# Kernel optimization log

Measured on AMD Instinct MI355X. Metric: run time of the kernel, lower is better.

The kernel has to match this reference:

```python
import jax, jax.numpy as jnp
import numpy as np

B, S, E, H, DK, DV = 2, 2048, 1024, 16, 64, 64
NEG = -1e9


def setup_inputs() -> dict:
    key = jax.random.key(0)
    ks = jax.random.split(key, 12)
    s = 0.02
    return {
        "query": jax.random.normal(ks[0], (B, S, E), jnp.float32),
        "key": jax.random.normal(ks[1], (B, S, E), jnp.float32),
        "value": jax.random.normal(ks[2], (B, S, E), jnp.float32),
        "mask": jax.random.randint(ks[3], (B, S, S), 0, 2, jnp.int32),
        "Wq": jax.random.normal(ks[4], (E, H * DK), jnp.float32) * s,
        "bq": jnp.zeros((H * DK,), jnp.float32),
        "Wk": jax.random.normal(ks[5], (E, H * DK), jnp.float32) * s,
        "bk": jnp.zeros((H * DK,), jnp.float32),
        "Wv": jax.random.normal(ks[6], (E, H * DV), jnp.float32) * s,
        "bv": jnp.zeros((H * DV,), jnp.float32),
        "Wo": jax.random.normal(ks[7], (H * DV, E), jnp.float32) * s,
        "bo": jnp.zeros((E,), jnp.float32),
    }


def reference(query, key, value, mask, Wq, bq, Wk, bk, Wv, bv, Wo, bo):
    # projections, then split heads: (B,S,H*D) -> (B,H,S,D)
    q = (query @ Wq + bq).reshape(B, S, H, DK).transpose(0, 2, 1, 3)
    k = (key @ Wk + bk).reshape(B, S, H, DK).transpose(0, 2, 1, 3)
    v = (value @ Wv + bv).reshape(B, S, H, DV).transpose(0, 2, 1, 3)
    scores = jnp.einsum("bhqd,bhkd->bhqk", q, k) / jnp.sqrt(jnp.float32(DK))
    scores = jnp.where(mask[:, None, :, :] == 0, jnp.float32(NEG), scores)
    weights = jax.nn.softmax(scores, axis=-1)
    ctx = jnp.einsum("bhqk,bhkd->bhqd", weights, v)
    ctx = ctx.transpose(0, 2, 1, 3).reshape(B, S, H * DV)
    return ctx @ Wo + bo
```

## Files before the change

### kernel.cpp

```cpp
#include <hip/hip_runtime.h>

typedef __attribute__((ext_vector_type(8))) short s16x8;
typedef __attribute__((ext_vector_type(4))) float f32x4;
typedef __attribute__((ext_vector_type(16))) float f32x16;
typedef unsigned short u16;
typedef unsigned int u32;
typedef unsigned long long u64;

__device__ __forceinline__ u16 f2bf(float f) {
  u32 u = __builtin_bit_cast(u32, f);
  u += 0x7fff + ((u >> 16) & 1);
  return (u16)(u >> 16);
}

__device__ __forceinline__ float exp2fast(float x) {
#if __has_builtin(__builtin_amdgcn_exp2f)
  return __builtin_amdgcn_exp2f(x);
#else
  return __expf(x * 0.6931471805599453f);
#endif
}

__device__ __forceinline__ void gload16(const void* g, void* l) {
  __builtin_amdgcn_global_load_lds((const __attribute__((address_space(1))) u32*)g,
                                   (__attribute__((address_space(3))) u32*)l, 16, 0, 0);
}

#define MFMA(a, b, c) __builtin_amdgcn_mfma_f32_16x16x32_bf16((a), (b), (c), 0, 0, 0)
#define MFMA32(a, b, c) __builtin_amdgcn_mfma_f32_32x32x16_bf16((a), (b), (c), 0, 0, 0)

#define QSCALE 0.18033688011112042f

__global__ __launch_bounds__(256) void prep(
    const float* __restrict__ q, const float* __restrict__ k, const float* __restrict__ v,
    u16* __restrict__ oq, u16* __restrict__ ok, u16* __restrict__ ov,
    const float* __restrict__ W0, const float* __restrict__ W1,
    const float* __restrict__ W2, const float* __restrict__ W3,
    u16* __restrict__ T0, u16* __restrict__ T1, u16* __restrict__ T2, u16* __restrict__ T3,
    const int* __restrict__ mask, u64* __restrict__ mb) {
  __shared__ float t[32][33];
  const int bx = blockIdx.x, tid = threadIdx.x;
  if (bx < 6144) {
    int z = bx >> 11;
    const float* src = (z == 0) ? q : (z == 1) ? k : v;
    u16* dst = (z == 0) ? oq : (z == 1) ? ok : ov;
    int i = (bx & 2047) * 256 + tid;
    const float4* s4 = (const float4*)src;
    float4 a = s4[2 * i], bb = s4[2 * i + 1];
    uint4 o;
    o.x = (u32)f2bf(a.x) | ((u32)f2bf(a.y) << 16);
    o.y = (u32)f2bf(a.z) | ((u32)f2bf(a.w) << 16);
    o.z = (u32)f2bf(bb.x) | ((u32)f2bf(bb.y) << 16);
    o.w = (u32)f2bf(bb.z) | ((u32)f2bf(bb.w) << 16);
    ((uint4*)dst)[i] = o;
  } else if (bx < 10240) {
    int r = bx - 6144;
    int z = r >> 10, t2 = r & 1023;
    const float* W = (z == 0) ? W0 : (z == 1) ? W1 : (z == 2) ? W2 : W3;
    u16* WT = (z == 0) ? T0 : (z == 1) ? T1 : (z == 2) ? T2 : T3;
    int nb = t2 & 31, kb = t2 >> 5;
    int tx = tid & 31, ty = tid >> 5;
    int n = nb * 32 + tx;
#pragma unroll
    for (int j = 0; j < 4; j++) {
      int kk = kb * 32 + ty + 8 * j;
      t[ty + 8 * j][tx] = W[(size_t)kk * 1024 + n];
    }
    __syncthreads();
    int kk = kb * 32 + tx;
#pragma unroll
    for (int j = 0; j < 4; j++) {
      int n2 = nb * 32 + ty + 8 * j;
      WT[(size_t)n2 * 1024 + kk] = f2bf(t[tx][ty + 8 * j]);
    }
  } else {
    int wi = (bx - 10240) * 4 + (tid >> 6);
    int lane = tid & 63;
    u64 bits = __ballot(mask[((size_t)wi << 6) + lane] != 0);
    if (lane == 0) mb[wi] = bits;
  }
}

template <int BM, int BN>
__device__ __forceinline__ void gemm_core(const u16* __restrict__ A, const u16* __restrict__ BT,
                                          int m0, int n0, u16* Ash, u16* Bsh,
                                          f32x4 (&acc)[BM / 32][BN / 32]) {
  constexpr int MF = BM / 32, NF = BN / 32;
  constexpr int BATCH = BM / 32 + BN / 32;
  const int tid = threadIdx.x;
  const int lane = tid & 63, wid = tid >> 6;
  const int r16 = lane & 15, g = lane >> 4;
  const int wm = wid >> 1, wn = wid & 1;
  const int swz = r16 & 7;
  const f32x4 vz = {0.f, 0.f, 0.f, 0.f};
#pragma unroll
  for (int mf = 0; mf < MF; mf++)
#pragma unroll
    for (int nf = 0; nf < NF; nf++) acc[mf][nf] = vz;

  auto stage = [&](int buf, int k0) {
#pragma unroll
    for (int i = 0; i < MF; i++) {
      int ch = i * 256 + tid;
      int row = ch >> 3, sc = (ch & 7) ^ (row & 7);
      gload16(A + (((size_t)(m0 + row)) << 10) + k0 + sc * 8,
              Ash + (size_t)buf * (BM * 64) + ch * 8);
    }
#pragma unroll
    for (int i = 0; i < NF; i++) {
      int ch = i * 256 + tid;
      int row = ch >> 3, sc = (ch & 7) ^ (row & 7);
      gload16(BT + (((size_t)(n0 + row)) << 10) + k0 + sc * 8,
              Bsh + (size_t)buf * (BN * 64) + ch * 8);
    }
  };

  asm volatile("" ::: "memory");
  stage(0, 0);
  asm volatile("" ::: "memory");
  stage(1, 64);
  asm volatile("" ::: "memory");

  for (int t = 0; t < 16; t++) {
    const int cur = t & 1;
    if (t == 15) {
      asm volatile("s_waitcnt vmcnt(0)" ::: "memory");
    } else if constexpr (BATCH == 8) {
      asm volatile("s_waitcnt vmcnt(8)" ::: "memory");
    } else {
      asm volatile("s_waitcnt vmcnt(6)" ::: "memory");
    }
    asm volatile("s_barrier" ::: "memory");

    const u16* Acur = Ash + (size_t)cur * (BM * 64);
    const u16* Bcur = Bsh + (size_t)cur * (BN * 64);
    __builtin_amdgcn_s_setprio(1);
#pragma unroll
    for (int kk = 0; kk < 2; kk++) {
      const int c = (kk * 4 + g);
      s16x8 af[MF], bfr[NF];
#pragma unroll
      for (int mf = 0; mf < MF; mf++)
        af[mf] = *(const s16x8*)(Acur + ((wm * (BM / 2) + mf * 16 + r16) << 6) +
                                 ((c ^ swz) << 3));
#pragma unroll
      for (int nf = 0; nf < NF; nf++)
        bfr[nf] = *(const s16x8*)(Bcur + ((wn * (BN / 2) + nf * 16 + r16) << 6) +
                                  ((c ^ swz) << 3));
#pragma unroll
      for (int mf = 0; mf < MF; mf++)
#pragma unroll
        for (int nf = 0; nf < NF; nf++) acc[mf][nf] = MFMA(af[mf], bfr[nf], acc[mf][nf]);
    }
    __builtin_amdgcn_s_setprio(0);

    asm volatile("s_barrier" ::: "memory");
    if (t + 2 < 16) stage(cur, (t + 2) * 64);
  }
}

__global__ __launch_bounds__(256, 2) void proj_gemm(
    const u16* __restrict__ Xq, const u16* __restrict__ Xk, const u16* __restrict__ Xv,
    const u16* __restrict__ WqT, const u16* __restrict__ WkT, const u16* __restrict__ WvT,
    const float* __restrict__ bq, const float* __restrict__ bk, const float* __restrict__ bv,
    u16* __restrict__ Qo, u16* __restrict__ Ko, u16* __restrict__ Vto) {
  __shared__ u16 Ash[2 * 128 * 64], Bsh[2 * 128 * 64];
  const int z = blockIdx.z;
  const u16* A = (z == 0) ? Xq : (z == 1) ? Xk : Xv;
  const u16* BT = (z == 0) ? WqT : (z == 1) ? WkT : WvT;
  const float* bias = (z == 0) ? bq : (z == 1) ? bk : bv;
  u16* O = (z == 0) ? Qo : (z == 1) ? Ko : Vto;
  const float sc = (z == 0) ? QSCALE : 1.0f;
  const int m0 = blockIdx.y * 128, n0 = blockIdx.x * 128;
  f32x4 acc[4][4];
  gemm_core<128, 128>(A, BT, m0, n0, Ash, Bsh, acc);
  const int tid = threadIdx.x, lane = tid & 63, wid = tid >> 6;
  const int r16 = lane & 15, g = lane >> 4, wm = wid >> 1, wn = wid & 1;
#pragma unroll
  for (int nf = 0; nf < 4; nf++) {
    int col = n0 + wn * 64 + nf * 16 + r16;
    float bb = bias[col];
    int h = col >> 6, d = col & 63;
#pragma unroll
    for (int mf = 0; mf < 4; mf++) {
#pragma unroll
      for (int ri = 0; ri < 4; ri++) {
        int row = m0 + wm * 64 + mf * 16 + g * 4 + ri;
        int b_ = row >> 11, s_ = row & 2047;
        u16 val = f2bf((acc[mf][nf][ri] + bb) * sc);
        if (z < 2)
          O[((((size_t)b_ * 16 + h) * 2048 + s_) << 6) + d] = val;
        else
          O[((((size_t)b_ * 16 + h) * 64 + d) << 11) + s_] = val;
      }
    }
  }
}

__global__ __launch_bounds__(256, 2) void out_gemm(const u16* __restrict__ ctx,
                                                   const u16* __restrict__ WoT,
                                                   const float* __restrict__ bo,
                                                   float* __restrict__ out) {
  __shared__ u16 Ash[2 * 64 * 64], Bsh[2 * 128 * 64];
  const int m0 = blockIdx.y * 64, n0 = blockIdx.x * 128;
  f32x4 acc[2][4];
  gemm_core<64, 128>(ctx, WoT, m0, n0, Ash, Bsh, acc);
  const int tid = threadIdx.x, lane = tid & 63, wid = tid >> 6;
  const int r16 = lane & 15, g = lane >> 4, wm = wid >> 1, wn = wid & 1;
#pragma unroll
  for (int nf = 0; nf < 4; nf++) {
    int col = n0 + wn * 64 + nf * 16 + r16;
    float bb = bo[col];
#pragma unroll
    for (int mf = 0; mf < 2; mf++) {
#pragma unroll
      for (int ri = 0; ri < 4; ri++) {
        int row = m0 + wm * 32 + mf * 16 + g * 4 + ri;
        out[((size_t)row << 10) + col] = acc[mf][nf][ri] + bb;
      }
    }
  }
}

__device__ __forceinline__ s16x8 pack4u(u32 a0, u32 a1, u32 b0, u32 b1) {
  union { u32 u[4]; s16x8 v; } p;
  p.u[0] = a0; p.u[1] = a1; p.u[2] = b0; p.u[3] = b1;
  return p.v;
}

__device__ __forceinline__ void softpack(const f32x16& sv, u32 wm, s16x8& pA, s16x8& pB) {
  float e[16];
#pragma unroll
  for (int qd = 0; qd < 4; qd++)
#pragma unroll
    for (int j = 0; j < 4; j++) {
      const int bit = qd * 8 + j;
      float ex = exp2fast(sv[qd * 4 + j]);
      u32 sext = (u32)(((int)(wm << (31 - bit))) >> 31);
      e[qd * 4 + j] = __builtin_bit_cast(float, __builtin_bit_cast(u32, ex) & sext);
    }
#pragma unroll
  for (int n = 0; n < 2; n++) {
    u32 a0, a1, b0, b1;
    asm("v_cvt_pk_bf16_f32 %0, %1, %2" : "=v"(a0) : "v"(e[n * 8 + 0]), "v"(e[n * 8 + 1]));
    asm("v_cvt_pk_bf16_f32 %0, %1, %2" : "=v"(a1) : "v"(e[n * 8 + 2]), "v"(e[n * 8 + 3]));
    asm("v_cvt_pk_bf16_f32 %0, %1, %2" : "=v"(b0) : "v"(e[n * 8 + 4]), "v"(e[n * 8 + 5]));
    asm("v_cvt_pk_bf16_f32 %0, %1, %2" : "=v"(b1) : "v"(e[n * 8 + 6]), "v"(e[n * 8 + 7]));
    asm("v_permlane32_swap_b32 %0, %1" : "+v"(a0), "+v"(b0));
    asm("v_permlane32_swap_b32 %0, %1" : "+v"(a1), "+v"(b1));
    if (n == 0) pA = pack4u(a0, a1, b0, b1);
    else        pB = pack4u(a0, a1, b0, b1);
  }
}

__global__ __launch_bounds__(256, 2) void flash_attn(const u16* __restrict__ Q,
                                                     const u16* __restrict__ K,
                                                     const u16* __restrict__ Vt,
                                                     const u64* __restrict__ Mb64,
                                                     u16* __restrict__ ctx) {
  __shared__ __align__(16) u16 Ksh[4][64][64];
  __shared__ __align__(16) u16 Vsh[4][64][64];

  const int tid = threadIdx.x, w = tid >> 6, lane = tid & 63;
  const int l31 = lane & 31, h5 = lane >> 5, l7 = lane & 7;

  int work = ((int)blockIdx.x & 7) * 64 + ((int)blockIdx.x >> 3);
  const int qt = work & 15, bh = work >> 4;
  const int b = bh >> 4, h = bh & 15;
  const int q0 = qt * 128 + w * 32;

  const u16* Qb = Q + ((size_t)bh << 17);
  const u16* Kb = K + ((size_t)bh << 17);
  const u16* Vb = Vt + ((size_t)bh << 17);
  const u64* Mrow = Mb64 + ((size_t)(b * 2048 + q0 + l31) << 5);

  const int srow = tid >> 3, sk16 = tid & 7;
#define STAGE(buf, kv0)                                                                   \
  {                                                                                       \
    _Pragma("unroll") for (int i = 0; i < 2; i++) {                                       \
      int row = i * 32 + srow;                                                            \
      int sc = sk16 ^ (row & 7);                                                          \
      gload16(Kb + (((size_t)((kv0) + row)) << 6) + sc * 8,                               \
              (char*)&Ksh[buf][0][0] + (i * 256 + tid) * 16);                             \
      gload16(Vb + (((size_t)row) << 11) + (kv0) + sc * 8,                                \
              (char*)&Vsh[buf][0][0] + (i * 256 + tid) * 16);                             \
    }                                                                                     \
  }

  s16x8 aq[4];
#pragma unroll
  for (int dk = 0; dk < 4; dk++)
    aq[dk] = *(const s16x8*)(Qb + ((q0 + l31) << 6) + dk * 16 + h5 * 8);
  asm volatile("" ::: "memory");
  STAGE(0, 0);
  STAGE(1, 64);
  u64 m_c0 = Mrow[0], m_c1 = Mrow[1];
  asm volatile("" ::: "memory");
  STAGE(2, 128);
  STAGE(3, 192);
  u64 m_n0 = Mrow[2], m_n1 = Mrow[3];
  asm volatile("" ::: "memory");

  s16x8 vones;
#pragma unroll
  for (int j = 0; j < 8; j++) vones[j] = (short)0x3F80;

  f32x16 o0, o1, o4;
#pragma unroll
  for (int r = 0; r < 16; r++) { o0[r] = 0.f; o1[r] = 0.f; o4[r] = 0.f; }

  for (int t = 0; t < 16; t++) {
    const int base = (t & 1) * 2;
    if (t == 15) {
      asm volatile("s_waitcnt vmcnt(0)" ::: "memory");
    } else {
      asm volatile("s_waitcnt vmcnt(10)" ::: "memory");
    }
    asm volatile("s_barrier" ::: "memory");

    const u16* KcA = &Ksh[base][0][0];
    const u16* KcB = &Ksh[base + 1][0][0];
    const u16* VcA = &Vsh[base][0][0];
    const u16* VcB = &Vsh[base + 1][0][0];

    f32x16 s0, s1, s2, s3;
#pragma unroll
    for (int r = 0; r < 16; r++) { s0[r] = 0.f; s1[r] = 0.f; s2[r] = 0.f; s3[r] = 0.f; }
    __builtin_amdgcn_s_setprio(1);
#pragma unroll
    for (int dk = 0; dk < 4; dk++) {
      int ch = (((dk << 1) + h5) ^ l7) << 3;
      s16x8 akA0 = *(const s16x8*)(KcA + (l31 << 6) + ch);
      s16x8 akA1 = *(const s16x8*)(KcA + ((32 + l31) << 6) + ch);
      s16x8 akB0 = *(const s16x8*)(KcB + (l31 << 6) + ch);
      s16x8 akB1 = *(const s16x8*)(KcB + ((32 + l31) << 6) + ch);
      s0 = MFMA32(akA0, aq[dk], s0);
      s1 = MFMA32(akA1, aq[dk], s1);
      s2 = MFMA32(akB0, aq[dk], s2);
      s3 = MFMA32(akB1, aq[dk], s3);
    }
    __builtin_amdgcn_s_setprio(0);

    u64 mshA = m_c0 >> (h5 << 2);
    s16x8 pa[4];
    softpack(s0, (u32)mshA, pa[0], pa[1]);
    softpack(s1, (u32)(mshA >> 32), pa[2], pa[3]);
    __builtin_amdgcn_s_setprio(1);
#pragma unroll
    for (int km = 0; km < 4; km++) {
      int ch = (((km << 1) + h5) ^ l7) << 3;
      s16x8 bv0 = *(const s16x8*)(VcA + (l31 << 6) + ch);
      s16x8 bv1 = *(const s16x8*)(VcA + ((32 + l31) << 6) + ch);
      o0 = MFMA32(pa[km], bv0, o0);
      o1 = MFMA32(pa[km], bv1, o1);
      o4 = MFMA32(pa[km], vones, o4);
    }
    __builtin_amdgcn_s_setprio(0);

    u64 mshB = m_c1 >> (h5 << 2);
    s16x8 pb[4];
    softpack(s2, (u32)mshB, pb[0], pb[1]);
    softpack(s3, (u32)(mshB >> 32), pb[2], pb[3]);
    __builtin_amdgcn_s_setprio(1);
#pragma unroll
    for (int km = 0; km < 4; km++) {
      int ch = (((km << 1) + h5) ^ l7) << 3;
      s16x8 bv0 = *(const s16x8*)(VcB + (l31 << 6) + ch);
      s16x8 bv1 = *(const s16x8*)(VcB + ((32 + l31) << 6) + ch);
      o0 = MFMA32(pb[km], bv0, o0);
      o1 = MFMA32(pb[km], bv1, o1);
      o4 = MFMA32(pb[km], vones, o4);
    }
    __builtin_amdgcn_s_setprio(0);

    asm volatile("s_barrier" ::: "memory");
    u64 mw0 = 0, mw1 = 0;
    if (t + 2 < 16) {
      STAGE(base, (2 * t + 4) * 64);
      STAGE(base + 1, (2 * t + 5) * 64);
      mw0 = Mrow[2 * t + 4];
      mw1 = Mrow[2 * t + 5];
    }
    m_c0 = m_n0; m_c1 = m_n1;
    m_n0 = mw0;  m_n1 = mw1;
  }
#undef STAGE

#pragma unroll
  for (int r = 0; r < 16; r++) {
    int qr = (r & 3) + 8 * (r >> 2) + 4 * h5;
    size_t rowoff = ((size_t)((b << 11) + q0 + qr)) << 10;
    float iv = 1.f / o4[r];
    ctx[rowoff + (h << 6) + l31]      = f2bf(o0[r] * iv);
    ctx[rowoff + (h << 6) + 32 + l31] = f2bf(o1[r] * iv);
  }
}

extern "C" void kernel_launch(void* const* d_in, const int* in_sizes, int n_in,
                              void* d_out, int out_size, void* d_ws, size_t ws_size,
                              hipStream_t stream) {
  const float* query = (const float*)d_in[0];
  const float* key_  = (const float*)d_in[1];
  const float* value = (const float*)d_in[2];
  const int*   mask  = (const int*)d_in[3];
  const float* Wq = (const float*)d_in[4];
  const float* bq = (const float*)d_in[5];
  const float* Wk = (const float*)d_in[6];
  const float* bk = (const float*)d_in[7];
  const float* Wv = (const float*)d_in[8];
  const float* bv = (const float*)d_in[9];
  const float* Wo = (const float*)d_in[10];
  const float* bo = (const float*)d_in[11];

  const size_t MB = 1048576;
  char* ws = (char*)d_ws;
  u16* Xq  = (u16*)(ws + 0 * MB);
  u16* Xk  = (u16*)(ws + 8 * MB);
  u16* Xv  = (u16*)(ws + 16 * MB);
  u16* WqT = (u16*)(ws + 24 * MB);
  u16* WkT = (u16*)(ws + 26 * MB);
  u16* WvT = (u16*)(ws + 28 * MB);
  u16* WoT = (u16*)(ws + 30 * MB);
  u16* Qd  = (u16*)(ws + 32 * MB);
  u16* Kd  = (u16*)(ws + 40 * MB);
  u16* Vtd = (u16*)(ws + 48 * MB);
  u16* ctx = (u16*)(ws + 56 * MB);
  u64* Mb  = (u64*)(ws + 72 * MB);

  prep<<<43008, 256, 0, stream>>>(query, key_, value, Xq, Xk, Xv,
                                  Wq, Wk, Wv, Wo, WqT, WkT, WvT, WoT, mask, Mb);

  proj_gemm<<<dim3(8, 32, 3), 256, 0, stream>>>(Xq, Xk, Xv, WqT, WkT, WvT, bq, bk, bv,
                                                Qd, Kd, Vtd);
  flash_attn<<<512, 256, 0, stream>>>(Qd, Kd, Vtd, Mb, ctx);
  out_gemm<<<dim3(8, 64), 256, 0, stream>>>(ctx, WoT, bo, (float*)d_out);
}
```

Baseline: 152.0 us.

## Split KV range across two wave groups per block with LDS partial reduction

Flash attention blocks now run 512 threads: two groups of four waves each process half of the KV sequence for the same 128 query rows, each with its own double-buffered K/V LDS region. The unnormalized partial outputs and row sums are combined through LDS before the final normalize-and-store. The mask bitmap layout is transposed so that each tile's mask words for consecutive query rows sit contiguously. This roughly doubles resident waves to hide latency, at the cost of a cross-group reduction, more LDS per block, and a shallower prefetch.

```diff
diff --git a/kernel.cpp b/kernel.cpp
--- a/kernel.cpp
+++ b/kernel.cpp
@@ -77,7 +77,10 @@
     int wi = (bx - 10240) * 4 + (tid >> 6);
     int lane = tid & 63;
     u64 bits = __ballot(mask[((size_t)wi << 6) + lane] != 0);
-    if (lane == 0) mb[wi] = bits;
+    if (lane == 0) {
+      int b_ = wi >> 16, q_ = (wi >> 5) & 2047, t_ = wi & 31;
+      mb[((size_t)b_ << 16) + ((size_t)t_ << 11) + q_] = bits;
+    }
   }
 }
 
@@ -253,37 +256,42 @@
   }
 }
 
-__global__ __launch_bounds__(256, 2) void flash_attn(const u16* __restrict__ Q,
+__global__ __launch_bounds__(512, 4) void flash_attn(const u16* __restrict__ Q,
                                                      const u16* __restrict__ K,
                                                      const u16* __restrict__ Vt,
                                                      const u64* __restrict__ Mb64,
                                                      u16* __restrict__ ctx) {
-  __shared__ __align__(16) u16 Ksh[4][64][64];
-  __shared__ __align__(16) u16 Vsh[4][64][64];
-
+  __shared__ __align__(16) char pool[65536];
   const int tid = threadIdx.x, w = tid >> 6, lane = tid & 63;
   const int l31 = lane & 31, h5 = lane >> 5, l7 = lane & 7;
+  const int g4 = w >> 2;
+  const int gt = tid & 255;
+
+  u16* Ksh = (u16*)(pool + g4 * 32768);
+  u16* Vsh = (u16*)(pool + g4 * 32768 + 16384);
 
   int work = ((int)blockIdx.x & 7) * 64 + ((int)blockIdx.x >> 3);
   const int qt = work & 15, bh = work >> 4;
   const int b = bh >> 4, h = bh & 15;
-  const int q0 = qt * 128 + w * 32;
+  const int q0 = qt * 128 + (w & 3) * 32;
 
   const u16* Qb = Q + ((size_t)bh << 17);
   const u16* Kb = K + ((size_t)bh << 17);
   const u16* Vb = Vt + ((size_t)bh << 17);
-  const u64* Mrow = Mb64 + ((size_t)(b * 2048 + q0 + l31) << 5);
-
-  const int srow = tid >> 3, sk16 = tid & 7;
+  const u64* MrowT = Mb64 + ((size_t)b << 16) + (q0 + l31);
+  const int w0 = g4 * 16;
+  const int kvb = g4 * 1024;
+
+  const int srow = gt >> 3, sk16 = gt & 7;
 #define STAGE(buf, kv0)                                                                   \
   {                                                                                       \
     _Pragma("unroll") for (int i = 0; i < 2; i++) {                                       \
       int row = i * 32 + srow;                                                            \
       int sc = sk16 ^ (row & 7);                                                          \
       gload16(Kb + (((size_t)((kv0) + row)) << 6) + sc * 8,                               \
-              (char*)&Ksh[buf][0][0] + (i * 256 + tid) * 16);                             \
+              (char*)Ksh + ((buf) * 512 + i * 256 + gt) * 16);                            \
       gload16(Vb + (((size_t)row) << 11) + (kv0) + sc * 8,                                \
-              (char*)&Vsh[buf][0][0] + (i * 256 + tid) * 16);                             \
+              (char*)Vsh + ((buf) * 512 + i * 256 + gt) * 16);                            \
     }                                                                                     \
   }
 
@@ -292,13 +300,11 @@
   for (int dk = 0; dk < 4; dk++)
     aq[dk] = *(const s16x8*)(Qb + ((q0 + l31) << 6) + dk * 16 + h5 * 8);
   asm volatile("" ::: "memory");
-  STAGE(0, 0);
-  STAGE(1, 64);
-  u64 m_c0 = Mrow[0], m_c1 = Mrow[1];
-  asm volatile("" ::: "memory");
-  STAGE(2, 128);
-  STAGE(3, 192);
-  u64 m_n0 = Mrow[2], m_n1 = Mrow[3];
+  STAGE(0, kvb);
+  u64 m_c = MrowT[(size_t)(w0 + 0) << 11];
+  asm volatile("" ::: "memory");
+  STAGE(1, kvb + 64);
+  u64 m_n = MrowT[(size_t)(w0 + 1) << 11];
   asm volatile("" ::: "memory");
 
   s16x8 vones;
@@ -310,89 +316,89 @@
   for (int r = 0; r < 16; r++) { o0[r] = 0.f; o1[r] = 0.f; o4[r] = 0.f; }
 
   for (int t = 0; t < 16; t++) {
-    const int base = (t & 1) * 2;
+    const int cur = t & 1;
     if (t == 15) {
       asm volatile("s_waitcnt vmcnt(0)" ::: "memory");
     } else {
-      asm volatile("s_waitcnt vmcnt(10)" ::: "memory");
+      asm volatile("s_waitcnt vmcnt(5)" ::: "memory");
     }
     asm volatile("s_barrier" ::: "memory");
 
-    const u16* KcA = &Ksh[base][0][0];
-    const u16* KcB = &Ksh[base + 1][0][0];
-    const u16* VcA = &Vsh[base][0][0];
-    const u16* VcB = &Vsh[base + 1][0][0];
-
-    f32x16 s0, s1, s2, s3;
-#pragma unroll
-    for (int r = 0; r < 16; r++) { s0[r] = 0.f; s1[r] = 0.f; s2[r] = 0.f; s3[r] = 0.f; }
+    const u16* Kc = Ksh + cur * 4096;
+    const u16* Vc = Vsh + cur * 4096;
+
+    f32x16 s0, s1;
+#pragma unroll
+    for (int r = 0; r < 16; r++) { s0[r] = 0.f; s1[r] = 0.f; }
     __builtin_amdgcn_s_setprio(1);
 #pragma unroll
     for (int dk = 0; dk < 4; dk++) {
       int ch = (((dk << 1) + h5) ^ l7) << 3;
-      s16x8 akA0 = *(const s16x8*)(KcA + (l31 << 6) + ch);
-      s16x8 akA1 = *(const s16x8*)(KcA + ((32 + l31) << 6) + ch);
-      s16x8 akB0 = *(const s16x8*)(KcB + (l31 << 6) + ch);
-      s16x8 akB1 = *(const s16x8*)(KcB + ((32 + l31) << 6) + ch);
-      s0 = MFMA32(akA0, aq[dk], s0);
-      s1 = MFMA32(akA1, aq[dk], s1);
-      s2 = MFMA32(akB0, aq[dk], s2);
-      s3 = MFMA32(akB1, aq[dk], s3);
+      s16x8 ak0 = *(const s16x8*)(Kc + (l31 << 6) + ch);
+      s16x8 ak1 = *(const s16x8*)(Kc + ((32 + l31) << 6) + ch);
+      s0 = MFMA32(ak0, aq[dk], s0);
+      s1 = MFMA32(ak1, aq[dk], s1);
     }
     __builtin_amdgcn_s_setprio(0);
 
-    u64 mshA = m_c0 >> (h5 << 2);
+    u64 msh = m_c >> (h5 << 2);
     s16x8 pa[4];
-    softpack(s0, (u32)mshA, pa[0], pa[1]);
-    softpack(s1, (u32)(mshA >> 32), pa[2], pa[3]);
+    softpack(s0, (u32)msh, pa[0], pa[1]);
+    softpack(s1, (u32)(msh >> 32), pa[2], pa[3]);
+
     __builtin_amdgcn_s_setprio(1);
 #pragma unroll
     for (int km = 0; km < 4; km++) {
       int ch = (((km << 1) + h5) ^ l7) << 3;
-      s16x8 bv0 = *(const s16x8*)(VcA + (l31 << 6) + ch);
-      s16x8 bv1 = *(const s16x8*)(VcA + ((32 + l31) << 6) + ch);
+      s16x8 bv0 = *(const s16x8*)(Vc + (l31 << 6) + ch);
+      s16x8 bv1 = *(const s16x8*)(Vc + ((32 + l31) << 6) + ch);
       o0 = MFMA32(pa[km], bv0, o0);
       o1 = MFMA32(pa[km], bv1, o1);
       o4 = MFMA32(pa[km], vones, o4);
     }
     __builtin_amdgcn_s_setprio(0);
 
-    u64 mshB = m_c1 >> (h5 << 2);
-    s16x8 pb[4];
-    softpack(s2, (u32)mshB, pb[0], pb[1]);
-    softpack(s3, (u32)(mshB >> 32), pb[2], pb[3]);
-    __builtin_amdgcn_s_setprio(1);
-#pragma unroll
-    for (int km = 0; km < 4; km++) {
-      int ch = (((km << 1) + h5) ^ l7) << 3;
-      s16x8 bv0 = *(const s16x8*)(VcB + (l31 << 6) + ch);
-      s16x8 bv1 = *(const s16x8*)(VcB + ((32 + l31) << 6) + ch);
-      o0 = MFMA32(pb[km], bv0, o0);
-      o1 = MFMA32(pb[km], bv1, o1);
-      o4 = MFMA32(pb[km], vones, o4);
-    }
-    __builtin_amdgcn_s_setprio(0);
-
     asm volatile("s_barrier" ::: "memory");
-    u64 mw0 = 0, mw1 = 0;
+    u64 m_new = 0;
     if (t + 2 < 16) {
-      STAGE(base, (2 * t + 4) * 64);
-      STAGE(base + 1, (2 * t + 5) * 64);
-      mw0 = Mrow[2 * t + 4];
-      mw1 = Mrow[2 * t + 5];
-    }
-    m_c0 = m_n0; m_c1 = m_n1;
-    m_n0 = mw0;  m_n1 = mw1;
+      STAGE(cur, kvb + (t + 2) * 64);
+      m_new = MrowT[(size_t)(w0 + t + 2) << 11];
+    }
+    m_c = m_n;
+    m_n = m_new;
   }
 #undef STAGE
 
-#pragma unroll
-  for (int r = 0; r < 16; r++) {
-    int qr = (r & 3) + 8 * (r >> 2) + 4 * h5;
-    size_t rowoff = ((size_t)((b << 11) + q0 + qr)) << 10;
-    float iv = 1.f / o4[r];
-    ctx[rowoff + (h << 6) + l31]      = f2bf(o0[r] * iv);
-    ctx[rowoff + (h << 6) + 32 + l31] = f2bf(o1[r] * iv);
+  float* part = (float*)pool;
+  if (g4 == 1) {
+    float* dst = part + (((w & 3) * 64 + lane) * 48);
+#pragma unroll
+    for (int j = 0; j < 4; j++) {
+      *(float4*)(dst + j * 4)      = make_float4(o0[j * 4], o0[j * 4 + 1], o0[j * 4 + 2], o0[j * 4 + 3]);
+      *(float4*)(dst + 16 + j * 4) = make_float4(o1[j * 4], o1[j * 4 + 1], o1[j * 4 + 2], o1[j * 4 + 3]);
+      *(float4*)(dst + 32 + j * 4) = make_float4(o4[j * 4], o4[j * 4 + 1], o4[j * 4 + 2], o4[j * 4 + 3]);
+    }
+  }
+  __syncthreads();
+  if (g4 == 0) {
+    const float* src = part + (((w & 3) * 64 + lane) * 48);
+#pragma unroll
+    for (int j = 0; j < 4; j++) {
+      float4 p0 = *(const float4*)(src + j * 4);
+      float4 p1 = *(const float4*)(src + 16 + j * 4);
+      float4 p4 = *(const float4*)(src + 32 + j * 4);
+      o0[j * 4] += p0.x; o0[j * 4 + 1] += p0.y; o0[j * 4 + 2] += p0.z; o0[j * 4 + 3] += p0.w;
+      o1[j * 4] += p1.x; o1[j * 4 + 1] += p1.y; o1[j * 4 + 2] += p1.z; o1[j * 4 + 3] += p1.w;
+      o4[j * 4] += p4.x; o4[j * 4 + 1] += p4.y; o4[j * 4 + 2] += p4.z; o4[j * 4 + 3] += p4.w;
+    }
+#pragma unroll
+    for (int r = 0; r < 16; r++) {
+      int qr = (r & 3) + 8 * (r >> 2) + 4 * h5;
+      size_t rowoff = ((size_t)((b << 11) + q0 + qr)) << 10;
+      float iv = 1.f / o4[r];
+      ctx[rowoff + (h << 6) + l31]      = f2bf(o0[r] * iv);
+      ctx[rowoff + (h << 6) + 32 + l31] = f2bf(o1[r] * iv);
+    }
   }
 }
 
@@ -432,6 +438,6 @@
 
   proj_gemm<<<dim3(8, 32, 3), 256, 0, stream>>>(Xq, Xk, Xv, WqT, WkT, WvT, bq, bk, bv,
                                                 Qd, Kd, Vtd);
-  flash_attn<<<512, 256, 0, stream>>>(Qd, Kd, Vtd, Mb, ctx);
+  flash_attn<<<512, 512, 0, stream>>>(Qd, Kd, Vtd, Mb, ctx);
   out_gemm<<<dim3(8, 64), 256, 0, stream>>>(ctx, WoT, bo, (float*)d_out);
 }
```

Measured after the change: 153.6 us. About the same (+1.0%).

## Move mask bit-packing into projection GEMM launch with transposed bitmask layout

Applied to the files above, without the earlier changes.

Mask ballot packing moves out of the prep kernel into an extra z-slice of the projection GEMM grid, so it can run alongside the GEMM tiles. Each 256-thread block now loops over 128 mask words per wave. The packed mask is stored transposed (batch, kv-tile, query), so the per-lane mask loads in flash attention hit consecutive addresses and coalesce. The risk is that the mask blocks, which do little work per block, compete with GEMM blocks for CUs and that the longer per-block loop adds latency.

```diff
diff --git a/kernel.cpp b/kernel.cpp
--- a/kernel.cpp
+++ b/kernel.cpp
@@ -36,8 +36,7 @@
     u16* __restrict__ oq, u16* __restrict__ ok, u16* __restrict__ ov,
     const float* __restrict__ W0, const float* __restrict__ W1,
     const float* __restrict__ W2, const float* __restrict__ W3,
-    u16* __restrict__ T0, u16* __restrict__ T1, u16* __restrict__ T2, u16* __restrict__ T3,
-    const int* __restrict__ mask, u64* __restrict__ mb) {
+    u16* __restrict__ T0, u16* __restrict__ T1, u16* __restrict__ T2, u16* __restrict__ T3) {
   __shared__ float t[32][33];
   const int bx = blockIdx.x, tid = threadIdx.x;
   if (bx < 6144) {
@@ -53,7 +52,7 @@
     o.z = (u32)f2bf(bb.x) | ((u32)f2bf(bb.y) << 16);
     o.w = (u32)f2bf(bb.z) | ((u32)f2bf(bb.w) << 16);
     ((uint4*)dst)[i] = o;
-  } else if (bx < 10240) {
+  } else {
     int r = bx - 6144;
     int z = r >> 10, t2 = r & 1023;
     const float* W = (z == 0) ? W0 : (z == 1) ? W1 : (z == 2) ? W2 : W3;
@@ -73,11 +72,6 @@
       int n2 = nb * 32 + ty + 8 * j;
       WT[(size_t)n2 * 1024 + kk] = f2bf(t[tx][ty + 8 * j]);
     }
-  } else {
-    int wi = (bx - 10240) * 4 + (tid >> 6);
-    int lane = tid & 63;
-    u64 bits = __ballot(mask[((size_t)wi << 6) + lane] != 0);
-    if (lane == 0) mb[wi] = bits;
   }
 }
 
@@ -163,9 +157,24 @@
     const u16* __restrict__ Xq, const u16* __restrict__ Xk, const u16* __restrict__ Xv,
     const u16* __restrict__ WqT, const u16* __restrict__ WkT, const u16* __restrict__ WvT,
     const float* __restrict__ bq, const float* __restrict__ bk, const float* __restrict__ bv,
-    u16* __restrict__ Qo, u16* __restrict__ Ko, u16* __restrict__ Vto) {
+    u16* __restrict__ Qo, u16* __restrict__ Ko, u16* __restrict__ Vto,
+    const int* __restrict__ mask, u64* __restrict__ mb) {
   __shared__ u16 Ash[2 * 128 * 64], Bsh[2 * 128 * 64];
   const int z = blockIdx.z;
+  if (z == 3) {
+    int m = blockIdx.y * 8 + blockIdx.x;
+    int w = threadIdx.x >> 6, lane = threadIdx.x & 63;
+#pragma unroll 4
+    for (int j = 0; j < 128; j++) {
+      int wi = (m * 4 + w) * 128 + j;
+      u64 bits = __ballot(mask[((size_t)wi << 6) + lane] != 0);
+      if (lane == 0) {
+        int b_ = wi >> 16, q_ = (wi >> 5) & 2047, t_ = wi & 31;
+        mb[((size_t)b_ << 16) + ((size_t)t_ << 11) + q_] = bits;
+      }
+    }
+    return;
+  }
   const u16* A = (z == 0) ? Xq : (z == 1) ? Xk : Xv;
   const u16* BT = (z == 0) ? WqT : (z == 1) ? WkT : WvT;
   const float* bias = (z == 0) ? bq : (z == 1) ? bk : bv;
@@ -272,7 +281,7 @@
   const u16* Qb = Q + ((size_t)bh << 17);
   const u16* Kb = K + ((size_t)bh << 17);
   const u16* Vb = Vt + ((size_t)bh << 17);
-  const u64* Mrow = Mb64 + ((size_t)(b * 2048 + q0 + l31) << 5);
+  const u64* MrowT = Mb64 + ((size_t)b << 16) + (q0 + l31);
 
   const int srow = tid >> 3, sk16 = tid & 7;
 #define STAGE(buf, kv0)                                                                   \
@@ -294,11 +303,11 @@
   asm volatile("" ::: "memory");
   STAGE(0, 0);
   STAGE(1, 64);
-  u64 m_c0 = Mrow[0], m_c1 = Mrow[1];
+  u64 m_c0 = MrowT[0], m_c1 = MrowT[(size_t)1 << 11];
   asm volatile("" ::: "memory");
   STAGE(2, 128);
   STAGE(3, 192);
-  u64 m_n0 = Mrow[2], m_n1 = Mrow[3];
+  u64 m_n0 = MrowT[(size_t)2 << 11], m_n1 = MrowT[(size_t)3 << 11];
   asm volatile("" ::: "memory");
 
   s16x8 vones;
@@ -378,8 +387,8 @@
     if (t + 2 < 16) {
       STAGE(base, (2 * t + 4) * 64);
       STAGE(base + 1, (2 * t + 5) * 64);
-      mw0 = Mrow[2 * t + 4];
-      mw1 = Mrow[2 * t + 5];
+      mw0 = MrowT[(size_t)(2 * t + 4) << 11];
+      mw1 = MrowT[(size_t)(2 * t + 5) << 11];
     }
     m_c0 = m_n0; m_c1 = m_n1;
     m_n0 = mw0;  m_n1 = mw1;
@@ -427,11 +436,11 @@
   u16* ctx = (u16*)(ws + 56 * MB);
   u64* Mb  = (u64*)(ws + 72 * MB);
 
-  prep<<<43008, 256, 0, stream>>>(query, key_, value, Xq, Xk, Xv,
-                                  Wq, Wk, Wv, Wo, WqT, WkT, WvT, WoT, mask, Mb);
-
-  proj_gemm<<<dim3(8, 32, 3), 256, 0, stream>>>(Xq, Xk, Xv, WqT, WkT, WvT, bq, bk, bv,
-                                                Qd, Kd, Vtd);
+  prep<<<10240, 256, 0, stream>>>(query, key_, value, Xq, Xk, Xv,
+                                  Wq, Wk, Wv, Wo, WqT, WkT, WvT, WoT);
+
+  proj_gemm<<<dim3(8, 32, 4), 256, 0, stream>>>(Xq, Xk, Xv, WqT, WkT, WvT, bq, bk, bv,
+                                                Qd, Kd, Vtd, mask, Mb);
   flash_attn<<<512, 256, 0, stream>>>(Qd, Kd, Vtd, Mb, ctx);
   out_gemm<<<dim3(8, 64), 256, 0, stream>>>(ctx, WoT, bo, (float*)d_out);
 }
```

Result: slower. 160.4 us (+5.5%).
